# Kernel tuning notes

Hardware: AMD Instinct MI355X
Metric: run time of the kernel (lower is better)

## Reference

```python
import jax, jax.numpy as jnp
import numpy as np

L, N, D, V, K = 512, 65536, 128, 21, 9  # seq len, n mutations, hidden, vocab, conv kernel


def setup_inputs() -> dict:
    key = jax.random.key(0)
    ks = jax.random.split(key, 24)
    # wildtype sequence and single-point mutants (guaranteed one mismatch each)
    wt = jax.random.randint(ks[0], (L,), 0, V, dtype=jnp.int32)
    pos = jax.random.randint(ks[1], (N,), 0, L)
    delta = jax.random.randint(ks[2], (N,), 1, V)
    muts = jnp.tile(wt[None, :], (N, 1))
    muts = muts.at[jnp.arange(N), pos].set(((wt[pos] + delta) % V).astype(jnp.int32))

    def lin(k, o, i):
        return jax.random.normal(k, (o, i), dtype=jnp.float32) / np.float32(np.sqrt(i))

    return {
        "all_input": jax.random.normal(ks[3], (L, D), dtype=jnp.float32),
        "seqs": wt[None, :],                      # [1, L]
        "sortcery_seqs": muts[None],              # [1, N, L]
        "sortcery_nrgs": jax.random.normal(ks[4], (1, N), dtype=jnp.float32),
        # LightAttention conv weights (torch Conv1d layout [out, in, k])
        "Wf": jax.random.normal(ks[5], (D, D, K), dtype=jnp.float32) / np.float32(np.sqrt(D * K)),
        "bf": jnp.zeros((D,), jnp.float32),
        "Wa": jax.random.normal(ks[6], (D, D, K), dtype=jnp.float32) / np.float32(np.sqrt(D * K)),
        "ba": jnp.zeros((D,), jnp.float32),
        # MLP: ReLU->Linear chain, sizes 128->128->64->32->21 (torch layout [out, in])
        "W1": lin(ks[7], 128, 128), "b1": jnp.zeros((128,), jnp.float32),
        "W2": lin(ks[8], 64, 128),  "b2": jnp.zeros((64,), jnp.float32),
        "W3": lin(ks[9], 32, 64),   "b3": jnp.zeros((32,), jnp.float32),
        "W4": lin(ks[10], 21, 32),  "b4": jnp.zeros((21,), jnp.float32),
        # ddg_out: Linear(1,1)
        "Wd": jax.random.normal(ks[11], (1, 1), dtype=jnp.float32),
        "bd": jnp.zeros((1,), jnp.float32),
    }


def _forward(all_input, sortcery_nrgs, Wf, bf, Wa, ba, W1, b1, W2, b2, W3, b3, W4, b4, Wd, bd,
             seqs, sortcery_seqs):
    wt = seqs[0]                                   # [L]
    muts = sortcery_seqs[0]                        # [N, L]
    mism = muts != wt[None, :]                     # [N, L]
    pos = jnp.argmax(mism, axis=1)                 # first mismatch position per mutation
    valid = jnp.any(mism, axis=1)                  # loop 'continue' when no mismatch

    x = all_input[pos]                             # [N, D] -- the length-1 conv input
    c = K // 2
    # Conv1d(k=9, pad=4) on a length-1 sequence: only the center tap sees nonzero input.
    feat = x @ Wf[:, :, c].T + bf                  # [N, D]
    att = x @ Wa[:, :, c].T + ba                   # [N, D]
    # softmax over the length-1 sequence axis is identically 1
    p = jax.nn.softmax(att[..., None], axis=-1)[..., 0]
    h = feat * p

    for W, b in ((W1, b1), (W2, b2), (W3, b3), (W4, b4)):
        h = jnp.maximum(h, 0.0) @ W.T + b
    logits = h                                     # [N, V]

    ddg_out = logits * Wd[0, 0] + bd[0]            # Linear(1,1) applied elementwise: [N, V]
    wc = wt[pos]                                   # wildtype char at mismatch
    mc = jnp.take_along_axis(muts, pos[:, None], axis=1)[:, 0]  # mutant char
    ddg = (jnp.take_along_axis(ddg_out, wc[:, None], axis=1)
           - jnp.take_along_axis(ddg_out, mc[:, None], axis=1))[:, 0]  # [N]

    preds = jnp.where(valid, ddg, 0.0)
    reals = jnp.where(valid, sortcery_nrgs[0], 0.0)
    return preds, reals


def reference(all_input, seqs, sortcery_seqs, sortcery_nrgs, Wf, bf, Wa, ba,
              W1, b1, W2, b2, W3, b3, W4, b4, Wd, bd):
    return _forward(all_input, sortcery_nrgs, Wf, bf, Wa, ba,
                    W1, b1, W2, b2, W3, b3, W4, b4, Wd, bd, seqs, sortcery_seqs)
```

## Files before the change

kernel.cpp:

```cpp
#include <hip/hip_runtime.h>

#define LSEQ 512
#define NMUT 65536
#define DDIM 128
#define VOCAB 21
#define KCONV 9
#define DDS 48
#define TPB2 2
#define NB_TAB (LSEQ / TPB2)
#define RPW 8
#define NB_SCAN (NMUT / (4 * RPW))
#define W4OFF 2080

__global__ __launch_bounds__(256) void extract_kernel(
    const float* __restrict__ Wf, float* __restrict__ WfC)
{
    const int t = blockIdx.x * 256 + threadIdx.x;
    WfC[t] = Wf[t * KCONV + KCONV / 2];
}

__global__ __launch_bounds__(256) void tab_kernel(
    const float* __restrict__ all_input,
    const int*   __restrict__ wt,
    const float* __restrict__ WfC, const float* __restrict__ bf,
    const float* __restrict__ W1, const float* __restrict__ b1,
    const float* __restrict__ W2, const float* __restrict__ b2,
    const float* __restrict__ W3, const float* __restrict__ b3,
    const float* __restrict__ W4, const float* __restrict__ b4,
    const float* __restrict__ Wd, const float* __restrict__ bd,
    float* __restrict__ tabDD)
{
    __shared__ float Wl[DDIM * 65];
    __shared__ float xa[DDIM][TPB2];
    __shared__ float xb[DDIM][TPB2];
    const int tid = threadIdx.x;
    const int p0  = blockIdx.x * TPB2;
    const int ph  = tid >> 7;
    const int o   = tid & 127;

    xa[o][ph] = all_input[(p0 + ph) * DDIM + o];

    float acc = bf[o];
    #pragma unroll
    for (int h = 0; h < 2; ++h) {
        __syncthreads();
        const float4* __restrict__ M4 = (const float4*)WfC;
        #pragma unroll
        for (int v = 0; v < 8; ++v) {
            const int vv  = tid + v * 256;
            const int row = vv >> 4, c4 = vv & 15;
            const float4 q = M4[row * 32 + h * 16 + c4];
            float* d = &Wl[row * 65 + c4 * 4];
            d[0] = q.x; d[1] = q.y; d[2] = q.z; d[3] = q.w;
        }
        __syncthreads();
        #pragma unroll 8
        for (int j = 0; j < 64; ++j)
            acc = fmaf(Wl[o * 65 + j], xa[h * 64 + j][ph], acc);
    }
    xb[o][ph] = fmaxf(acc, 0.f);

    acc = b1[o];
    #pragma unroll
    for (int h = 0; h < 2; ++h) {
        __syncthreads();
        const float4* __restrict__ M4 = (const float4*)W1;
        #pragma unroll
        for (int v = 0; v < 8; ++v) {
            const int vv  = tid + v * 256;
            const int row = vv >> 4, c4 = vv & 15;
            const float4 q = M4[row * 32 + h * 16 + c4];
            float* d = &Wl[row * 65 + c4 * 4];
            d[0] = q.x; d[1] = q.y; d[2] = q.z; d[3] = q.w;
        }
        __syncthreads();
        #pragma unroll 8
        for (int j = 0; j < 64; ++j)
            acc = fmaf(Wl[o * 65 + j], xb[h * 64 + j][ph], acc);
    }
    __syncthreads();
    xa[o][ph] = fmaxf(acc, 0.f);
    __syncthreads();

    {
        const float4* __restrict__ M4 = (const float4*)W2;
        #pragma unroll
        for (int v = 0; v < 8; ++v) {
            const int vv  = tid + v * 256;
            const int row = vv >> 5, c4 = vv & 31;
            const float4 q = M4[vv];
            float* d = &Wl[row * 129 + c4 * 4];
            d[0] = q.x; d[1] = q.y; d[2] = q.z; d[3] = q.w;
        }
    }
    __syncthreads();
    if (o < 64) {
        float a3 = b2[o];
        #pragma unroll 8
        for (int i = 0; i < 128; ++i)
            a3 = fmaf(Wl[o * 129 + i], xa[i][ph], a3);
        xb[o][ph] = fmaxf(a3, 0.f);
    }
    __syncthreads();

    if (tid < 512) {
        const int row = tid >> 4, c4 = tid & 15;
        const float4 q = ((const float4*)W3)[tid];
        float* d = &Wl[row * 65 + c4 * 4];
        d[0] = q.x; d[1] = q.y; d[2] = q.z; d[3] = q.w;
    } else if (tid < 512 + 168) {
        const int vv = tid - 512;
        const int row = vv >> 3, c4 = vv & 7;
        const float4 q = ((const float4*)W4)[vv];
        float* d = &Wl[W4OFF + row * 33 + c4 * 4];
        d[0] = q.x; d[1] = q.y; d[2] = q.z; d[3] = q.w;
    }
    __syncthreads();

    if (o < 32) {
        float a4 = b3[o];
        #pragma unroll 8
        for (int i = 0; i < 64; ++i)
            a4 = fmaf(Wl[o * 65 + i], xb[i][ph], a4);
        xa[o][ph] = fmaxf(a4, 0.f);
    }
    __syncthreads();

    if (o < VOCAB) {
        float a5 = b4[o];
        #pragma unroll
        for (int i = 0; i < 32; ++i)
            a5 = fmaf(Wl[W4OFF + o * 33 + i], xa[i][ph], a5);
        xb[o][ph] = a5 * Wd[0] + bd[0];
    }
    __syncthreads();

    if (tid < TPB2 * 41) {
        const int pl = tid / 41;
        const int j  = tid - pl * 41;
        const int wc = wt[p0 + pl];
        const int mc = wc + j - 20;
        float v = 0.f;
        if (mc >= 0 && mc < VOCAB)
            v = xb[wc][pl] - xb[mc][pl];
        tabDD[(p0 + pl) * DDS + j] = v;
    }
}

#define RESOLVE2(A, W, BP)                                                     \
    {                                                                          \
        const int dx = (A).x - (W).x, dy = (A).y - (W).y;                      \
        const unsigned long long msk = __ballot((dx | dy) != 0);               \
        if (msk) {                                                             \
            const int j = dx ? 0 : 1;                                          \
            const int d = dx ? dx : dy;                                        \
            const int cand = ((d + 32) << 10) | ((BP) + 2 * lane + j);         \
            res[k] = __shfl(cand, __ffsll(msk) - 1);                           \
        }                                                                      \
    }

__global__ __launch_bounds__(256) void scan_kernel(
    const int*   __restrict__ wt,
    const int*   __restrict__ muts,
    const float* __restrict__ nrgs,
    const float* __restrict__ tabDD,
    float* __restrict__ preds,
    float* __restrict__ reals)
{
    const int tid   = threadIdx.x;
    const int lane  = tid & 63;
    const int rbase = (blockIdx.x * 4 + (tid >> 6)) * RPW;

    const int2* __restrict__ wt2 = (const int2*)wt;
    const int2 w0 = wt2[lane];
    const int2 w1 = wt2[64 + lane];
    const int2 w2 = wt2[128 + lane];
    const int2 w3 = wt2[192 + lane];
    const int2* __restrict__ base = (const int2*)muts + (size_t)rbase * (LSEQ / 2);

    int res[RPW];
    int2 a[RPW];

    #pragma unroll
    for (int k = 0; k < RPW; ++k)
        a[k] = base[(size_t)k * (LSEQ / 2) + lane];
    #pragma unroll
    for (int k = 0; k < RPW; ++k) {
        res[k] = -1;
        RESOLVE2(a[k], w0, 0);
    }

    #pragma unroll
    for (int k = 0; k < RPW; ++k)
        if (res[k] < 0) a[k] = base[(size_t)k * (LSEQ / 2) + 64 + lane];
    #pragma unroll
    for (int k = 0; k < RPW; ++k)
        if (res[k] < 0) RESOLVE2(a[k], w1, 128);

    #pragma unroll
    for (int k = 0; k < RPW; ++k)
        if (res[k] < 0) a[k] = base[(size_t)k * (LSEQ / 2) + 128 + lane];
    #pragma unroll
    for (int k = 0; k < RPW; ++k)
        if (res[k] < 0) RESOLVE2(a[k], w2, 256);

    #pragma unroll
    for (int k = 0; k < RPW; ++k)
        if (res[k] < 0) a[k] = base[(size_t)k * (LSEQ / 2) + 192 + lane];
    #pragma unroll
    for (int k = 0; k < RPW; ++k)
        if (res[k] < 0) RESOLVE2(a[k], w3, 384);

    int myres = -1;
    #pragma unroll
    for (int k = 0; k < RPW; ++k)
        if (lane == k) myres = res[k];
    if (lane < RPW) {
        float pred = 0.f, real = 0.f;
        if (myres >= 0) {
            const int pos = myres & 1023;
            const int d0  = (myres >> 10) - 32;
            pred = tabDD[pos * DDS + d0 + 20];
            real = nrgs[rbase + lane];
        }
        preds[rbase + lane] = pred;
        reals[rbase + lane] = real;
    }
}

extern "C" void kernel_launch(void* const* d_in, const int* in_sizes, int n_in,
                              void* d_out, int out_size, void* d_ws, size_t ws_size,
                              hipStream_t stream) {
    const float* all_input = (const float*)d_in[0];
    const int*   seqs      = (const int*)  d_in[1];
    const int*   muts      = (const int*)  d_in[2];
    const float* nrgs      = (const float*)d_in[3];
    const float* Wf        = (const float*)d_in[4];
    const float* bf        = (const float*)d_in[5];
    const float* W1 = (const float*)d_in[8];
    const float* b1 = (const float*)d_in[9];
    const float* W2 = (const float*)d_in[10];
    const float* b2 = (const float*)d_in[11];
    const float* W3 = (const float*)d_in[12];
    const float* b3 = (const float*)d_in[13];
    const float* W4 = (const float*)d_in[14];
    const float* b4 = (const float*)d_in[15];
    const float* Wd = (const float*)d_in[16];
    const float* bd = (const float*)d_in[17];

    char* ws = (char*)d_ws;
    float* WfC   = (float*)ws;  ws += DDIM * DDIM * 4;
    float* tabDD = (float*)ws;
    float* preds = (float*)d_out;
    float* reals = (float*)d_out + NMUT;

    extract_kernel<<<DDIM * DDIM / 256, 256, 0, stream>>>(Wf, WfC);

    tab_kernel<<<NB_TAB, 256, 0, stream>>>(
        all_input, seqs, WfC, bf, W1, b1, W2, b2, W3, b3, W4, b4, Wd, bd,
        tabDD);

    scan_kernel<<<NB_SCAN, 256, 0, stream>>>(
        seqs, muts, nrgs, tabDD, preds, reals);
}
```

Measured before the change: 36.11 us.

## Run table build and mutation scan concurrently in one fused launch

The center-tap weight extraction is folded into the table-building path, and the table builder and mismatch scan are merged into a single launch with disjoint block ranges. Each table block now handles 8 positions instead of 2 and uses float4 accumulators, so weight staging is amortized over more positions. The scan writes a packed position/delta code to a workspace, and a small third kernel does the table lookup and writes outputs. This removes a serialized dependency so the memory-bound scan can overlap the table compute, at the cost of an extra launch and an extra round-trip through the meta buffer.

```diff
diff --git a/kernel.cpp b/kernel.cpp
--- a/kernel.cpp
+++ b/kernel.cpp
@@ -6,146 +6,11 @@
 #define VOCAB 21
 #define KCONV 9
 #define DDS 48
-#define TPB2 2
-#define NB_TAB (LSEQ / TPB2)
+#define TPB 8
+#define NB_TAB (LSEQ / TPB)
 #define RPW 8
 #define NB_SCAN (NMUT / (4 * RPW))
 #define W4OFF 2080
-
-__global__ __launch_bounds__(256) void extract_kernel(
-    const float* __restrict__ Wf, float* __restrict__ WfC)
-{
-    const int t = blockIdx.x * 256 + threadIdx.x;
-    WfC[t] = Wf[t * KCONV + KCONV / 2];
-}
-
-__global__ __launch_bounds__(256) void tab_kernel(
-    const float* __restrict__ all_input,
-    const int*   __restrict__ wt,
-    const float* __restrict__ WfC, const float* __restrict__ bf,
-    const float* __restrict__ W1, const float* __restrict__ b1,
-    const float* __restrict__ W2, const float* __restrict__ b2,
-    const float* __restrict__ W3, const float* __restrict__ b3,
-    const float* __restrict__ W4, const float* __restrict__ b4,
-    const float* __restrict__ Wd, const float* __restrict__ bd,
-    float* __restrict__ tabDD)
-{
-    __shared__ float Wl[DDIM * 65];
-    __shared__ float xa[DDIM][TPB2];
-    __shared__ float xb[DDIM][TPB2];
-    const int tid = threadIdx.x;
-    const int p0  = blockIdx.x * TPB2;
-    const int ph  = tid >> 7;
-    const int o   = tid & 127;
-
-    xa[o][ph] = all_input[(p0 + ph) * DDIM + o];
-
-    float acc = bf[o];
-    #pragma unroll
-    for (int h = 0; h < 2; ++h) {
-        __syncthreads();
-        const float4* __restrict__ M4 = (const float4*)WfC;
-        #pragma unroll
-        for (int v = 0; v < 8; ++v) {
-            const int vv  = tid + v * 256;
-            const int row = vv >> 4, c4 = vv & 15;
-            const float4 q = M4[row * 32 + h * 16 + c4];
-            float* d = &Wl[row * 65 + c4 * 4];
-            d[0] = q.x; d[1] = q.y; d[2] = q.z; d[3] = q.w;
-        }
-        __syncthreads();
-        #pragma unroll 8
-        for (int j = 0; j < 64; ++j)
-            acc = fmaf(Wl[o * 65 + j], xa[h * 64 + j][ph], acc);
-    }
-    xb[o][ph] = fmaxf(acc, 0.f);
-
-    acc = b1[o];
-    #pragma unroll
-    for (int h = 0; h < 2; ++h) {
-        __syncthreads();
-        const float4* __restrict__ M4 = (const float4*)W1;
-        #pragma unroll
-        for (int v = 0; v < 8; ++v) {
-            const int vv  = tid + v * 256;
-            const int row = vv >> 4, c4 = vv & 15;
-            const float4 q = M4[row * 32 + h * 16 + c4];
-            float* d = &Wl[row * 65 + c4 * 4];
-            d[0] = q.x; d[1] = q.y; d[2] = q.z; d[3] = q.w;
-        }
-        __syncthreads();
-        #pragma unroll 8
-        for (int j = 0; j < 64; ++j)
-            acc = fmaf(Wl[o * 65 + j], xb[h * 64 + j][ph], acc);
-    }
-    __syncthreads();
-    xa[o][ph] = fmaxf(acc, 0.f);
-    __syncthreads();
-
-    {
-        const float4* __restrict__ M4 = (const float4*)W2;
-        #pragma unroll
-        for (int v = 0; v < 8; ++v) {
-            const int vv  = tid + v * 256;
-            const int row = vv >> 5, c4 = vv & 31;
-            const float4 q = M4[vv];
-            float* d = &Wl[row * 129 + c4 * 4];
-            d[0] = q.x; d[1] = q.y; d[2] = q.z; d[3] = q.w;
-        }
-    }
-    __syncthreads();
-    if (o < 64) {
-        float a3 = b2[o];
-        #pragma unroll 8
-        for (int i = 0; i < 128; ++i)
-            a3 = fmaf(Wl[o * 129 + i], xa[i][ph], a3);
-        xb[o][ph] = fmaxf(a3, 0.f);
-    }
-    __syncthreads();
-
-    if (tid < 512) {
-        const int row = tid >> 4, c4 = tid & 15;
-        const float4 q = ((const float4*)W3)[tid];
-        float* d = &Wl[row * 65 + c4 * 4];
-        d[0] = q.x; d[1] = q.y; d[2] = q.z; d[3] = q.w;
-    } else if (tid < 512 + 168) {
-        const int vv = tid - 512;
-        const int row = vv >> 3, c4 = vv & 7;
-        const float4 q = ((const float4*)W4)[vv];
-        float* d = &Wl[W4OFF + row * 33 + c4 * 4];
-        d[0] = q.x; d[1] = q.y; d[2] = q.z; d[3] = q.w;
-    }
-    __syncthreads();
-
-    if (o < 32) {
-        float a4 = b3[o];
-        #pragma unroll 8
-        for (int i = 0; i < 64; ++i)
-            a4 = fmaf(Wl[o * 65 + i], xb[i][ph], a4);
-        xa[o][ph] = fmaxf(a4, 0.f);
-    }
-    __syncthreads();
-
-    if (o < VOCAB) {
-        float a5 = b4[o];
-        #pragma unroll
-        for (int i = 0; i < 32; ++i)
-            a5 = fmaf(Wl[W4OFF + o * 33 + i], xa[i][ph], a5);
-        xb[o][ph] = a5 * Wd[0] + bd[0];
-    }
-    __syncthreads();
-
-    if (tid < TPB2 * 41) {
-        const int pl = tid / 41;
-        const int j  = tid - pl * 41;
-        const int wc = wt[p0 + pl];
-        const int mc = wc + j - 20;
-        float v = 0.f;
-        if (mc >= 0 && mc < VOCAB)
-            v = xb[wc][pl] - xb[mc][pl];
-        tabDD[(p0 + pl) * DDS + j] = v;
-    }
-}
 
 #define RESOLVE2(A, W, BP)                                                     \
     {                                                                          \
@@ -159,17 +24,182 @@
         }                                                                      \
     }
 
-__global__ __launch_bounds__(256) void scan_kernel(
+__global__ __launch_bounds__(256) void fused_kernel(
+    const float* __restrict__ all_input,
     const int*   __restrict__ wt,
     const int*   __restrict__ muts,
-    const float* __restrict__ nrgs,
-    const float* __restrict__ tabDD,
-    float* __restrict__ preds,
-    float* __restrict__ reals)
+    const float* __restrict__ Wf, const float* __restrict__ bf,
+    const float* __restrict__ W1, const float* __restrict__ b1,
+    const float* __restrict__ W2, const float* __restrict__ b2,
+    const float* __restrict__ W3, const float* __restrict__ b3,
+    const float* __restrict__ W4, const float* __restrict__ b4,
+    const float* __restrict__ Wd, const float* __restrict__ bd,
+    float* __restrict__ tabDD,
+    int*   __restrict__ meta)
 {
-    const int tid   = threadIdx.x;
+    __shared__ float Wl[4224];
+    __shared__ float xa[DDIM][TPB];
+    __shared__ float xb[DDIM][TPB];
+    const int tid = threadIdx.x;
+
+    if (blockIdx.x < NB_TAB) {
+        const int p0 = blockIdx.x * TPB;
+        const int ph = tid >> 7;
+        const int o  = tid & 127;
+
+        #pragma unroll
+        for (int k = 0; k < 4; ++k) {
+            const int f = tid + k * 256;
+            xa[f & 127][f >> 7] = all_input[p0 * DDIM + f];
+        }
+
+        float4 acc;
+        { const float b = bf[o]; acc = make_float4(b, b, b, b); }
+        #pragma unroll
+        for (int q = 0; q < 4; ++q) {
+            __syncthreads();
+            #pragma unroll
+            for (int it = 0; it < 16; ++it) {
+                const int e = tid + it * 256;
+                const int row = e >> 5, col = e & 31;
+                Wl[row * 33 + col] =
+                    Wf[(row * DDIM + q * 32 + col) * KCONV + KCONV / 2];
+            }
+            __syncthreads();
+            #pragma unroll
+            for (int j = 0; j < 32; ++j) {
+                const float w = Wl[o * 33 + j];
+                const float4 x = *(const float4*)&xa[q * 32 + j][ph * 4];
+                acc.x = fmaf(x.x, w, acc.x);
+                acc.y = fmaf(x.y, w, acc.y);
+                acc.z = fmaf(x.z, w, acc.z);
+                acc.w = fmaf(x.w, w, acc.w);
+            }
+        }
+        xb[o][ph * 4 + 0] = fmaxf(acc.x, 0.f);
+        xb[o][ph * 4 + 1] = fmaxf(acc.y, 0.f);
+        xb[o][ph * 4 + 2] = fmaxf(acc.z, 0.f);
+        xb[o][ph * 4 + 3] = fmaxf(acc.w, 0.f);
+
+        { const float b = b1[o]; acc = make_float4(b, b, b, b); }
+        #pragma unroll
+        for (int q = 0; q < 4; ++q) {
+            __syncthreads();
+            #pragma unroll
+            for (int it = 0; it < 16; ++it) {
+                const int e = tid + it * 256;
+                const int row = e >> 5, col = e & 31;
+                Wl[row * 33 + col] = W1[row * DDIM + q * 32 + col];
+            }
+            __syncthreads();
+            #pragma unroll
+            for (int j = 0; j < 32; ++j) {
+                const float w = Wl[o * 33 + j];
+                const float4 x = *(const float4*)&xb[q * 32 + j][ph * 4];
+                acc.x = fmaf(x.x, w, acc.x);
+                acc.y = fmaf(x.y, w, acc.y);
+                acc.z = fmaf(x.z, w, acc.z);
+                acc.w = fmaf(x.w, w, acc.w);
+            }
+        }
+        xa[o][ph * 4 + 0] = fmaxf(acc.x, 0.f);
+        xa[o][ph * 4 + 1] = fmaxf(acc.y, 0.f);
+        xa[o][ph * 4 + 2] = fmaxf(acc.z, 0.f);
+        xa[o][ph * 4 + 3] = fmaxf(acc.w, 0.f);
+
+        float4 a3;
+        { const float b = (o < 64) ? b2[o] : 0.f; a3 = make_float4(b, b, b, b); }
+        #pragma unroll
+        for (int h = 0; h < 2; ++h) {
+            __syncthreads();
+            #pragma unroll
+            for (int it = 0; it < 16; ++it) {
+                const int e = tid + it * 256;
+                const int row = e >> 6, col = e & 63;
+                Wl[row * 65 + col] = W2[row * DDIM + h * 64 + col];
+            }
+            __syncthreads();
+            if (o < 64) {
+                #pragma unroll
+                for (int j = 0; j < 64; ++j) {
+                    const float w = Wl[o * 65 + j];
+                    const float4 x = *(const float4*)&xa[h * 64 + j][ph * 4];
+                    a3.x = fmaf(x.x, w, a3.x);
+                    a3.y = fmaf(x.y, w, a3.y);
+                    a3.z = fmaf(x.z, w, a3.z);
+                    a3.w = fmaf(x.w, w, a3.w);
+                }
+            }
+        }
+        if (o < 64) {
+            xb[o][ph * 4 + 0] = fmaxf(a3.x, 0.f);
+            xb[o][ph * 4 + 1] = fmaxf(a3.y, 0.f);
+            xb[o][ph * 4 + 2] = fmaxf(a3.z, 0.f);
+            xb[o][ph * 4 + 3] = fmaxf(a3.w, 0.f);
+        }
+        __syncthreads();
+
+        for (int e = tid; e < 2048; e += 256)
+            Wl[(e >> 6) * 65 + (e & 63)] = W3[e];
+        for (int e = tid; e < 672; e += 256)
+            Wl[W4OFF + (e >> 5) * 33 + (e & 31)] = W4[e];
+        __syncthreads();
+
+        if (o < 32) {
+            float4 a4;
+            { const float b = b3[o]; a4 = make_float4(b, b, b, b); }
+            #pragma unroll
+            for (int j = 0; j < 64; ++j) {
+                const float w = Wl[o * 65 + j];
+                const float4 x = *(const float4*)&xb[j][ph * 4];
+                a4.x = fmaf(x.x, w, a4.x);
+                a4.y = fmaf(x.y, w, a4.y);
+                a4.z = fmaf(x.z, w, a4.z);
+                a4.w = fmaf(x.w, w, a4.w);
+            }
+            xa[o][ph * 4 + 0] = fmaxf(a4.x, 0.f);
+            xa[o][ph * 4 + 1] = fmaxf(a4.y, 0.f);
+            xa[o][ph * 4 + 2] = fmaxf(a4.z, 0.f);
+            xa[o][ph * 4 + 3] = fmaxf(a4.w, 0.f);
+        }
+        __syncthreads();
+
+        if (o < VOCAB) {
+            const float wd = Wd[0], bdv = bd[0];
+            float4 a5;
+            { const float b = b4[o]; a5 = make_float4(b, b, b, b); }
+            #pragma unroll
+            for (int j = 0; j < 32; ++j) {
+                const float w = Wl[W4OFF + o * 33 + j];
+                const float4 x = *(const float4*)&xa[j][ph * 4];
+                a5.x = fmaf(x.x, w, a5.x);
+                a5.y = fmaf(x.y, w, a5.y);
+                a5.z = fmaf(x.z, w, a5.z);
+                a5.w = fmaf(x.w, w, a5.w);
+            }
+            xb[o][ph * 4 + 0] = a5.x * wd + bdv;
+            xb[o][ph * 4 + 1] = a5.y * wd + bdv;
+            xb[o][ph * 4 + 2] = a5.z * wd + bdv;
+            xb[o][ph * 4 + 3] = a5.w * wd + bdv;
+        }
+        __syncthreads();
+
+        for (int e = tid; e < TPB * 41; e += 256) {
+            const int pl = e / 41;
+            const int j  = e - pl * 41;
+            const int wc = wt[p0 + pl];
+            const int mc = wc + j - 20;
+            float v = 0.f;
+            if (mc >= 0 && mc < VOCAB)
+                v = xb[wc][pl] - xb[mc][pl];
+            tabDD[(p0 + pl) * DDS + j] = v;
+        }
+        return;
+    }
+
     const int lane  = tid & 63;
-    const int rbase = (blockIdx.x * 4 + (tid >> 6)) * RPW;
+    const int sbid  = blockIdx.x - NB_TAB;
+    const int rbase = (sbid * 4 + (tid >> 6)) * RPW;
 
     const int2* __restrict__ wt2 = (const int2*)wt;
     const int2 w0 = wt2[lane];
@@ -215,17 +245,28 @@
     #pragma unroll
     for (int k = 0; k < RPW; ++k)
         if (lane == k) myres = res[k];
-    if (lane < RPW) {
-        float pred = 0.f, real = 0.f;
-        if (myres >= 0) {
-            const int pos = myres & 1023;
-            const int d0  = (myres >> 10) - 32;
-            pred = tabDD[pos * DDS + d0 + 20];
-            real = nrgs[rbase + lane];
-        }
-        preds[rbase + lane] = pred;
-        reals[rbase + lane] = real;
+    if (lane < RPW)
+        meta[rbase + lane] = myres;
+}
+
+__global__ __launch_bounds__(256) void lookup_kernel(
+    const int*   __restrict__ meta,
+    const float* __restrict__ tabDD,
+    const float* __restrict__ nrgs,
+    float* __restrict__ preds,
+    float* __restrict__ reals)
+{
+    const int r = blockIdx.x * 256 + threadIdx.x;
+    const int m = meta[r];
+    float pred = 0.f, real = 0.f;
+    if (m >= 0) {
+        const int pos = m & 1023;
+        const int d0  = (m >> 10) - 32;
+        pred = tabDD[pos * DDS + d0 + 20];
+        real = nrgs[r];
     }
+    preds[r] = pred;
+    reals[r] = real;
 }
 
 extern "C" void kernel_launch(void* const* d_in, const int* in_sizes, int n_in,
@@ -249,17 +290,15 @@
     const float* bd = (const float*)d_in[17];
 
     char* ws = (char*)d_ws;
-    float* WfC   = (float*)ws;  ws += DDIM * DDIM * 4;
-    float* tabDD = (float*)ws;
+    float* tabDD = (float*)ws;  ws += LSEQ * DDS * 4;
+    int*   meta  = (int*)ws;
     float* preds = (float*)d_out;
     float* reals = (float*)d_out + NMUT;
 
-    extract_kernel<<<DDIM * DDIM / 256, 256, 0, stream>>>(Wf, WfC);
-
-    tab_kernel<<<NB_TAB, 256, 0, stream>>>(
-        all_input, seqs, WfC, bf, W1, b1, W2, b2, W3, b3, W4, b4, Wd, bd,
-        tabDD);
-
-    scan_kernel<<<NB_SCAN, 256, 0, stream>>>(
-        seqs, muts, nrgs, tabDD, preds, reals);
+    fused_kernel<<<NB_TAB + NB_SCAN, 256, 0, stream>>>(
+        all_input, seqs, muts,
+        Wf, bf, W1, b1, W2, b2, W3, b3, W4, b4, Wd, bd,
+        tabDD, meta);
+
+    lookup_kernel<<<NMUT / 256, 256, 0, stream>>>(meta, tabDD, nrgs, preds, reals);
 }
```

New measurement: 31.24 us, median of 2. 13.5% less time.
